# Kernel tuning notes

Measured on AMD Instinct MI355X. Metric: run time of the kernel, lower is better.

The kernel has to match this reference:

```python
import jax, jax.numpy as jnp
import numpy as np

NA = 3            # anchors per scale
NC = 80           # num classes
THRESH = 0.6      # wh-IoU anchor-match threshold
EPS = 1e-7

ANCHORS_PX = np.array([[12,16],[19,36],[40,28],[36,75],[76,55],[72,146],
                       [142,110],[192,243],[459,401]], dtype=np.float32).reshape(3, 3, 2)


def setup_inputs() -> dict:
    key = jax.random.key(0)
    k1, k2, k3, k4, k5, k6 = jax.random.split(key, 6)
    B, M = 16, 32
    p0 = jax.random.normal(k1, (B, NA * (5 + NC), 80, 80), jnp.float32)
    p1 = jax.random.normal(k2, (B, NA * (5 + NC), 40, 40), jnp.float32)
    p2 = jax.random.normal(k3, (B, NA * (5 + NC), 20, 20), jnp.float32)
    # targets: [B, M, 6] = (img_idx, class in [1,NC], cx, cy, w, h) normalized to [0,1]
    bidx = jnp.broadcast_to(jnp.arange(B, dtype=jnp.float32)[:, None], (B, M))
    cls = jax.random.randint(k4, (B, M), 1, NC + 1).astype(jnp.float32)
    xy = jax.random.uniform(k5, (B, M, 2), minval=0.05, maxval=0.95)
    ka, kj = jax.random.split(k6)
    aidx = jax.random.randint(ka, (B, M), 0, 9)
    base_wh = jnp.asarray(ANCHORS_PX.reshape(9, 2))[aidx] / 640.0
    jitter = jnp.exp(jax.random.uniform(kj, (B, M, 2), minval=-0.15, maxval=0.15))
    wh = base_wh * jitter
    targets = jnp.concatenate([bidx[..., None], cls[..., None], xy, wh], axis=-1)
    return {"p0": p0, "p1": p1, "p2": p2,
            "targets": targets,
            "anchors": jnp.asarray(ANCHORS_PX),
            "image_size": jnp.array([640.0, 640.0], jnp.float32)}


def _bce_logits(x, t):
    # BCEWithLogits, pos_weight=1, elementwise
    return jnp.maximum(x, 0.0) - x * t + jnp.log1p(jnp.exp(-jnp.abs(x)))


def _giou(pbox, tbox):
    # boxes [N,4] in cxcywh
    px1 = pbox[:, 0] - pbox[:, 2] * 0.5
    py1 = pbox[:, 1] - pbox[:, 3] * 0.5
    px2 = pbox[:, 0] + pbox[:, 2] * 0.5
    py2 = pbox[:, 1] + pbox[:, 3] * 0.5
    tx1 = tbox[:, 0] - tbox[:, 2] * 0.5
    ty1 = tbox[:, 1] - tbox[:, 3] * 0.5
    tx2 = tbox[:, 0] + tbox[:, 2] * 0.5
    ty2 = tbox[:, 1] + tbox[:, 3] * 0.5
    iw = jnp.clip(jnp.minimum(px2, tx2) - jnp.maximum(px1, tx1), 0.0)
    ih = jnp.clip(jnp.minimum(py2, ty2) - jnp.maximum(py1, ty1), 0.0)
    inter = iw * ih
    union = pbox[:, 2] * pbox[:, 3] + tbox[:, 2] * tbox[:, 3] - inter + EPS
    iou = inter / union
    cw = jnp.maximum(px2, tx2) - jnp.minimum(px1, tx1)
    ch = jnp.maximum(py2, ty2) - jnp.minimum(py1, ty1)
    c_area = cw * ch + EPS
    return iou - (c_area - union) / c_area


def _scale_losses(pi, tflat, anchors_i, image_size):
    # pi: [B, NA*(5+NC), H, W]; tflat: [N,6]; anchors_i: [NA,2] in pixels
    B = pi.shape[0]
    H, W = pi.shape[-2:]
    stride = image_size / jnp.array([H, W], jnp.float32)          # (sH, sW)
    anchor = anchors_i / stride[::-1][None, :]                    # anchors in grid units (w,h)
    gain = jnp.concatenate([jnp.ones((2,), jnp.float32),
                            (1.0 / stride)[jnp.array([1, 0, 1, 0])]])
    t = tflat * gain                                              # [N,6]
    gwh = t[:, 4:6]
    # wh-IoU matrix [NA, N] -> best anchor per target
    inter = (jnp.minimum(anchor[:, None, 0], gwh[None, :, 0])
             * jnp.minimum(anchor[:, None, 1], gwh[None, :, 1]))
    union = anchor[:, None, 0] * anchor[:, None, 1] + gwh[None, :, 0] * gwh[None, :, 1] - inter
    iou = inter / union
    best = iou.max(0)
    a = iou.argmax(0)
    mask = best > THRESH                                          # fixed-shape mask replaces torch boolean compaction
    maskf = mask.astype(jnp.float32)

    b = jnp.where(mask, t[:, 0].astype(jnp.int32), 0)
    c = t[:, 1].astype(jnp.int32)
    gxy = t[:, 2:4]
    gi = jnp.where(mask, gxy[:, 0].astype(jnp.int32), 0)
    gj = jnp.where(mask, gxy[:, 1].astype(jnp.int32), 0)
    a_s = jnp.where(mask, a, 0)

    pir = pi.reshape(B, NA, 5 + NC, H, W).transpose(0, 1, 3, 4, 2)  # [B,NA,H,W,5+NC]
    ps = pir[b, a_s, gj, gi]                                        # [N,5+NC]
    tobj = jnp.zeros((B, NA, H, W), jnp.float32)
    tobj = tobj.at[b, a_s, gj, gi].max(jax.lax.stop_gradient(maskf))

    pxy = jax.nn.sigmoid(ps[:, 0:2])
    pwh = jnp.minimum(jnp.exp(ps[:, 2:4]), 1000.0) * anchor[a_s]
    pbox = jnp.concatenate([pxy, pwh], 1)
    tbox = jnp.concatenate([gxy % 1.0, t[:, 4:6]], 1)
    giou = _giou(pbox, tbox)
    nb = jnp.maximum(maskf.sum(), 1.0)
    lbox = (maskf * (1.0 - giou)).sum() / nb
    tcls = jax.nn.one_hot(c - 1, NC, dtype=jnp.float32)             # cp=1, cn=0 (eps=0)
    lcls = (maskf[:, None] * _bce_logits(ps[:, 5:], tcls)).sum() / (nb * NC)
    lobj = _bce_logits(pir[..., 4], tobj).mean()
    return lbox, lobj, lcls


def _total_loss(p0, p1, p2, targets, anchors, image_size):
    tflat = targets.reshape(-1, 6)
    lbox = lobj = lcls = jnp.float32(0.0)
    for i, pi in enumerate([p0, p1, p2]):
        lb, lo, lc = _scale_losses(pi, tflat, anchors[i], image_size)
        lbox = lbox + lb
        lobj = lobj + lo
        lcls = lcls + lc
    lbox = lbox * 3.54
    lobj = lobj * 64.3
    lcls = lcls * 37.4
    return lbox + lobj + lcls, lbox, lobj, lcls


def reference(p0, p1, p2, targets, anchors, image_size):
    return _total_loss(p0, p1, p2, targets, anchors, image_size)
```

## Files before the change

### kernel.cpp

```cpp
#include <hip/hip_runtime.h>
#include <math.h>

#define NAANCH 3
#define NCLS 80
#define BATCH 16
#define NTGT 512
#define CH 85

#define V4_S0 76800
#define V4_S1 19200
#define V4_S2 4800
#define V4_TOT (V4_S0 + V4_S1 + V4_S2)
#define OBJ_BLOCKS 197

__device__ __forceinline__ float bce0(float x) {
    return fmaxf(x, 0.0f) + log1pf(expf(-fabsf(x)));
}

__device__ __forceinline__ float wave_sum(float v) {
    for (int off = 32; off > 0; off >>= 1) v += __shfl_down(v, off, 64);
    return v;
}

__global__ void fused_kernel(const float* __restrict__ p0,
                             const float* __restrict__ p1,
                             const float* __restrict__ p2,
                             const float* __restrict__ targets,
                             const float* __restrict__ anchors,
                             const float* __restrict__ image_size,
                             float* __restrict__ ws) {
    const int tid  = threadIdx.x;
    const int lane = tid & 63;
    const int wid  = tid >> 6;

    __shared__ int   sh_key[NTGT];
    __shared__ int   sh_off[NTGT];
    __shared__ int   sh_ci[NTGT];
    __shared__ unsigned char sh_mk[NTGT];
    __shared__ float red[4][8];

    if (blockIdx.x < 3) {
        const int s = blockIdx.x;
        const int j = tid;
        const int H = (s == 0) ? 80 : ((s == 1) ? 40 : 20);
        const int W = H;
        const int HW = H * W;
        const float* pi = (s == 0) ? p0 : ((s == 1) ? p1 : p2);

        const float stride0 = image_size[0] / (float)H;
        const float stride1 = image_size[1] / (float)W;
        const float gx = 1.0f / stride1;
        const float gy = 1.0f / stride0;

        const float t0 = targets[j * 6 + 0];
        const float t1 = targets[j * 6 + 1];
        const float tx = targets[j * 6 + 2] * gx;
        const float ty = targets[j * 6 + 3] * gy;
        const float gw = targets[j * 6 + 4] * gx;
        const float gh = targets[j * 6 + 5] * gy;

        float best = -1.0f; int abest = 0;
        for (int k = 0; k < NAANCH; ++k) {
            float aw = anchors[(s * NAANCH + k) * 2 + 0] / stride1;
            float ah = anchors[(s * NAANCH + k) * 2 + 1] / stride0;
            float inter = fminf(aw, gw) * fminf(ah, gh);
            float uni = aw * ah + gw * gh - inter;
            float iou = inter / uni;
            if (iou > best) { best = iou; abest = k; }
        }
        const bool  mask  = best > 0.6f;
        const float maskf = mask ? 1.0f : 0.0f;

        int b  = mask ? (int)t0 : 0;
        const int c = (int)t1;
        int gi = mask ? (int)tx : 0;
        int gj = mask ? (int)ty : 0;
        const int a_s = mask ? abest : 0;
        gi = min(max(gi, 0), W - 1);
        gj = min(max(gj, 0), H - 1);
        b  = min(max(b, 0), BATCH - 1);

        const int key = ((b * NAANCH + a_s) * H + gj) * W + gi;
        const int off = (b * (NAANCH * CH) + a_s * CH) * HW + gj * W + gi;

        float lbox_t = 0.0f, ps4 = 0.0f;
        if (mask) {
            const float ps0 = pi[off + 0 * HW];
            const float ps1 = pi[off + 1 * HW];
            const float ps2 = pi[off + 2 * HW];
            const float ps3 = pi[off + 3 * HW];
            ps4 = pi[off + 4 * HW];

            const float aw = anchors[(s * NAANCH + a_s) * 2 + 0] / stride1;
            const float ah = anchors[(s * NAANCH + a_s) * 2 + 1] / stride0;

            const float pxc = 1.0f / (1.0f + expf(-ps0));
            const float pyc = 1.0f / (1.0f + expf(-ps1));
            const float pw  = fminf(expf(ps2), 1000.0f) * aw;
            const float ph  = fminf(expf(ps3), 1000.0f) * ah;
            const float txc = tx - floorf(tx);
            const float tyc = ty - floorf(ty);

            const float px1 = pxc - pw * 0.5f, py1 = pyc - ph * 0.5f;
            const float px2 = pxc + pw * 0.5f, py2 = pyc + ph * 0.5f;
            const float qx1 = txc - gw * 0.5f, qy1 = tyc - gh * 0.5f;
            const float qx2 = txc + gw * 0.5f, qy2 = tyc + gh * 0.5f;
            const float iw = fmaxf(fminf(px2, qx2) - fmaxf(px1, qx1), 0.0f);
            const float ih = fmaxf(fminf(py2, qy2) - fmaxf(py1, qy1), 0.0f);
            const float inter = iw * ih;
            const float uni = pw * ph + gw * gh - inter + 1e-7f;
            const float iou = inter / uni;
            const float cw  = fmaxf(px2, qx2) - fminf(px1, qx1);
            const float chh = fmaxf(py2, qy2) - fminf(py1, qy1);
            const float carea = cw * chh + 1e-7f;
            lbox_t = 1.0f - (iou - (carea - uni) / carea);
        }

        sh_key[j] = key;
        sh_off[j] = off;
        sh_ci[j]  = c - 1;
        sh_mk[j]  = mask ? 1 : 0;
        __syncthreads();

        float corr = 0.0f;
        if (mask) {
            bool dup = false;
            for (int j2 = 0; j2 < j; ++j2)
                if (sh_mk[j2] && sh_key[j2] == key) { dup = true; break; }
            if (!dup) corr = -ps4;
        }

        float v0 = wave_sum(lbox_t);
        float v1 = wave_sum(maskf);
        float v2 = wave_sum(corr);
        if (lane == 0) { red[0][wid] = v0; red[1][wid] = v1; red[2][wid] = v2; }
        __syncthreads();

        float lcls_w = 0.0f;
        for (int j2 = wid; j2 < NTGT; j2 += 8) {
            if (!sh_mk[j2]) continue;
            const int toff = sh_off[j2];
            const int ci   = sh_ci[j2];
            const int k1 = lane;
            float x1 = pi[toff + (5 + k1) * HW];
            float c1 = bce0(x1) - ((k1 == ci) ? x1 : 0.0f);
            float c2 = 0.0f;
            if (lane < NCLS - 64) {
                const int k2 = 64 + lane;
                float x2 = pi[toff + (5 + k2) * HW];
                c2 = bce0(x2) - ((k2 == ci) ? x2 : 0.0f);
            }
            float tsum = wave_sum(c1 + c2);
            if (lane == 0) lcls_w += tsum;
        }
        if (lane == 0) red[3][wid] = lcls_w;
        __syncthreads();

        if (tid == 0) {
            float acc[4] = {0.f, 0.f, 0.f, 0.f};
            for (int w = 0; w < 8; ++w) {
                acc[0] += red[0][w]; acc[1] += red[1][w];
                acc[2] += red[2][w]; acc[3] += red[3][w];
            }
            ws[3 + s]  = acc[0];
            ws[6 + s]  = acc[1];
            ws[9 + s]  = acc[3];
            ws[12 + s] = acc[2];
        }
    } else {
        const int vb = (blockIdx.x - 3) * 512 + tid;
        float a0 = 0.f, a1 = 0.f, a2 = 0.f;
        if (vb < V4_TOT) {
            const float4* addr; int hw4; int sflag;
            if (vb < V4_S0) {
                const int u = vb;
                const int ba = u / 1600;  hw4 = u - ba * 1600;
                const int b = ba / 3, a = ba - 3 * b;
                addr = (const float4*)(p0 + (size_t)((b * NAANCH + a) * CH + 4) * 6400);
                sflag = 0;
            } else if (vb < V4_S0 + V4_S1) {
                const int u = vb - V4_S0;
                const int ba = u / 400;   hw4 = u - ba * 400;
                const int b = ba / 3, a = ba - 3 * b;
                addr = (const float4*)(p1 + (size_t)((b * NAANCH + a) * CH + 4) * 1600);
                sflag = 1;
            } else {
                const int u = vb - V4_S0 - V4_S1;
                const int ba = u / 100;   hw4 = u - ba * 100;
                const int b = ba / 3, a = ba - 3 * b;
                addr = (const float4*)(p2 + (size_t)((b * NAANCH + a) * CH + 4) * 400);
                sflag = 2;
            }
            float4 x = addr[hw4];
            float v = bce0(x.x) + bce0(x.y) + bce0(x.z) + bce0(x.w);
            if (sflag == 0) a0 = v; else if (sflag == 1) a1 = v; else a2 = v;
        }
        a0 = wave_sum(a0); a1 = wave_sum(a1); a2 = wave_sum(a2);
        if (lane == 0) { red[0][wid] = a0; red[1][wid] = a1; red[2][wid] = a2; }
        __syncthreads();
        if (tid == 0) {
            float s0 = 0.f, s1 = 0.f, s2 = 0.f;
            for (int w = 0; w < 8; ++w) { s0 += red[0][w]; s1 += red[1][w]; s2 += red[2][w]; }
            const int blk = blockIdx.x - 3;
            ws[16 + blk * 3 + 0] = s0;
            ws[16 + blk * 3 + 1] = s1;
            ws[16 + blk * 3 + 2] = s2;
        }
    }
}

__global__ void finalize_kernel(const float* __restrict__ ws, float* __restrict__ out) {
    const int t = threadIdx.x;
    const int lane = t & 63, wid = t >> 6;
    float o0 = 0.f, o1 = 0.f, o2 = 0.f;
    if (t < OBJ_BLOCKS) {
        o0 = ws[16 + t * 3 + 0];
        o1 = ws[16 + t * 3 + 1];
        o2 = ws[16 + t * 3 + 2];
    }
    o0 = wave_sum(o0); o1 = wave_sum(o1); o2 = wave_sum(o2);
    __shared__ float part[3][4];
    if (lane == 0) { part[0][wid] = o0; part[1][wid] = o1; part[2][wid] = o2; }
    __syncthreads();
    if (t == 0) {
        float obj[3];
        for (int s = 0; s < 3; ++s)
            obj[s] = part[s][0] + part[s][1] + part[s][2] + part[s][3];
        const float Ns[3] = { 307200.0f, 76800.0f, 19200.0f };
        float lbox = 0.f, lobj = 0.f, lcls = 0.f;
        for (int s = 0; s < 3; ++s) {
            float nb = fmaxf(ws[6 + s], 1.0f);
            lbox += ws[3 + s] / nb;
            lobj += (obj[s] + ws[12 + s]) / Ns[s];
            lcls += ws[9 + s] / (nb * (float)NCLS);
        }
        lbox *= 3.54f; lobj *= 64.3f; lcls *= 37.4f;
        out[0] = lbox + lobj + lcls;
        out[1] = lbox;
        out[2] = lobj;
        out[3] = lcls;
    }
}

extern "C" void kernel_launch(void* const* d_in, const int* in_sizes, int n_in,
                              void* d_out, int out_size, void* d_ws, size_t ws_size,
                              hipStream_t stream) {
    const float* p0       = (const float*)d_in[0];
    const float* p1       = (const float*)d_in[1];
    const float* p2       = (const float*)d_in[2];
    const float* targets  = (const float*)d_in[3];
    const float* anchors  = (const float*)d_in[4];
    const float* img_size = (const float*)d_in[5];
    float* out = (float*)d_out;
    float* ws  = (float*)d_ws;

    fused_kernel<<<3 + OBJ_BLOCKS, 512, 0, stream>>>(p0, p1, p2, targets, anchors, img_size, ws);
    finalize_kernel<<<1, 256, 0, stream>>>(ws, out);
}
```

Before: 155.0 us.

## Merge finalize into main kernel via cooperative grid sync and grid-stride loop

Replaces the two-kernel launch with one cooperative kernel that uses a grid-wide sync before a single block computes the final loss. The objectness blocks drop from 197 to 64 and use a grid-stride loop with accumulation. This removes one kernel launch and its gap, in exchange for grid-sync overhead and fewer blocks streaming the objectness channel. The target-matching blocks, which likely dominate, are unchanged, and cooperative launch limits grid size.

```diff
diff --git a/kernel.cpp b/kernel.cpp
--- a/kernel.cpp
+++ b/kernel.cpp
@@ -1,5 +1,8 @@
 #include <hip/hip_runtime.h>
+#include <hip/hip_cooperative_groups.h>
 #include <math.h>
+
+namespace cg = cooperative_groups;
 
 #define NAANCH 3
 #define NCLS 80
@@ -11,7 +14,8 @@
 #define V4_S1 19200
 #define V4_S2 4800
 #define V4_TOT (V4_S0 + V4_S1 + V4_S2)
-#define OBJ_BLOCKS 197
+#define OBJ_BLOCKS 64
+#define GRID_BLOCKS (3 + OBJ_BLOCKS)
 
 __device__ __forceinline__ float bce0(float x) {
     return fmaxf(x, 0.0f) + log1pf(expf(-fabsf(x)));
@@ -22,13 +26,14 @@
     return v;
 }
 
-__global__ void fused_kernel(const float* __restrict__ p0,
-                             const float* __restrict__ p1,
-                             const float* __restrict__ p2,
-                             const float* __restrict__ targets,
-                             const float* __restrict__ anchors,
-                             const float* __restrict__ image_size,
-                             float* __restrict__ ws) {
+__global__ void yolo_loss_kernel(const float* __restrict__ p0,
+                                 const float* __restrict__ p1,
+                                 const float* __restrict__ p2,
+                                 const float* __restrict__ targets,
+                                 const float* __restrict__ anchors,
+                                 const float* __restrict__ image_size,
+                                 float* __restrict__ ws,
+                                 float* __restrict__ out) {
     const int tid  = threadIdx.x;
     const int lane = tid & 63;
     const int wid  = tid >> 6;
@@ -168,9 +173,8 @@
             ws[12 + s] = acc[2];
         }
     } else {
-        const int vb = (blockIdx.x - 3) * 512 + tid;
         float a0 = 0.f, a1 = 0.f, a2 = 0.f;
-        if (vb < V4_TOT) {
+        for (int vb = (blockIdx.x - 3) * 512 + tid; vb < V4_TOT; vb += OBJ_BLOCKS * 512) {
             const float4* addr; int hw4; int sflag;
             if (vb < V4_S0) {
                 const int u = vb;
@@ -193,7 +197,7 @@
             }
             float4 x = addr[hw4];
             float v = bce0(x.x) + bce0(x.y) + bce0(x.z) + bce0(x.w);
-            if (sflag == 0) a0 = v; else if (sflag == 1) a1 = v; else a2 = v;
+            if (sflag == 0) a0 += v; else if (sflag == 1) a1 += v; else a2 += v;
         }
         a0 = wave_sum(a0); a1 = wave_sum(a1); a2 = wave_sum(a2);
         if (lane == 0) { red[0][wid] = a0; red[1][wid] = a1; red[2][wid] = a2; }
@@ -207,38 +211,31 @@
             ws[16 + blk * 3 + 2] = s2;
         }
     }
-}
-
-__global__ void finalize_kernel(const float* __restrict__ ws, float* __restrict__ out) {
-    const int t = threadIdx.x;
-    const int lane = t & 63, wid = t >> 6;
-    float o0 = 0.f, o1 = 0.f, o2 = 0.f;
-    if (t < OBJ_BLOCKS) {
-        o0 = ws[16 + t * 3 + 0];
-        o1 = ws[16 + t * 3 + 1];
-        o2 = ws[16 + t * 3 + 2];
-    }
-    o0 = wave_sum(o0); o1 = wave_sum(o1); o2 = wave_sum(o2);
-    __shared__ float part[3][4];
-    if (lane == 0) { part[0][wid] = o0; part[1][wid] = o1; part[2][wid] = o2; }
-    __syncthreads();
-    if (t == 0) {
-        float obj[3];
-        for (int s = 0; s < 3; ++s)
-            obj[s] = part[s][0] + part[s][1] + part[s][2] + part[s][3];
-        const float Ns[3] = { 307200.0f, 76800.0f, 19200.0f };
-        float lbox = 0.f, lobj = 0.f, lcls = 0.f;
-        for (int s = 0; s < 3; ++s) {
-            float nb = fmaxf(ws[6 + s], 1.0f);
-            lbox += ws[3 + s] / nb;
-            lobj += (obj[s] + ws[12 + s]) / Ns[s];
-            lcls += ws[9 + s] / (nb * (float)NCLS);
-        }
-        lbox *= 3.54f; lobj *= 64.3f; lcls *= 37.4f;
-        out[0] = lbox + lobj + lcls;
-        out[1] = lbox;
-        out[2] = lobj;
-        out[3] = lcls;
+
+    __threadfence();
+    cg::this_grid().sync();
+
+    if (blockIdx.x == 0 && tid < 64) {
+        float o0 = ws[16 + tid * 3 + 0];
+        float o1 = ws[16 + tid * 3 + 1];
+        float o2 = ws[16 + tid * 3 + 2];
+        o0 = wave_sum(o0); o1 = wave_sum(o1); o2 = wave_sum(o2);
+        if (tid == 0) {
+            const float obj[3] = { o0, o1, o2 };
+            const float Ns[3] = { 307200.0f, 76800.0f, 19200.0f };
+            float lbox = 0.f, lobj = 0.f, lcls = 0.f;
+            for (int s = 0; s < 3; ++s) {
+                float nb = fmaxf(ws[6 + s], 1.0f);
+                lbox += ws[3 + s] / nb;
+                lobj += (obj[s] + ws[12 + s]) / Ns[s];
+                lcls += ws[9 + s] / (nb * (float)NCLS);
+            }
+            lbox *= 3.54f; lobj *= 64.3f; lcls *= 37.4f;
+            out[0] = lbox + lobj + lcls;
+            out[1] = lbox;
+            out[2] = lobj;
+            out[3] = lcls;
+        }
     }
 }
 
@@ -254,6 +251,8 @@
     float* out = (float*)d_out;
     float* ws  = (float*)d_ws;
 
-    fused_kernel<<<3 + OBJ_BLOCKS, 512, 0, stream>>>(p0, p1, p2, targets, anchors, img_size, ws);
-    finalize_kernel<<<1, 256, 0, stream>>>(ws, out);
-}
+    void* args[] = { (void*)&p0, (void*)&p1, (void*)&p2, (void*)&targets,
+                     (void*)&anchors, (void*)&img_size, (void*)&ws, (void*)&out };
+    hipLaunchCooperativeKernel((void*)yolo_loss_kernel,
+                               dim3(GRID_BLOCKS), dim3(512), args, 0, stream);
+}
```

Result: slower. 198.1 us (+27.8%).
